# Performance work log

Hardware: AMD Instinct MI355X
Metric: run time of the kernel (lower is better)

Reference implementation:

```python
import jax, jax.numpy as jnp
import numpy as np
from jax.scipy.special import logsumexp

NUM_TAGS = 128
B, S = 256, 1024


def setup_inputs() -> dict:
    key = jax.random.key(0)
    k1, k2, k3, k4, k5 = jax.random.split(key, 5)
    emissions = jax.random.normal(k1, (B, S, NUM_TAGS), dtype=jnp.float32)
    masks = jnp.ones((B, S), dtype=jnp.float32)
    tags = jax.random.randint(k2, (B, S), 0, NUM_TAGS, dtype=jnp.int64)
    transitions = jax.random.normal(k3, (NUM_TAGS, NUM_TAGS), dtype=jnp.float32)
    start_transitions = jax.random.normal(k4, (NUM_TAGS,), dtype=jnp.float32)
    end_transitions = jax.random.normal(k5, (NUM_TAGS,), dtype=jnp.float32)
    return {"emissions": emissions, "masks": masks, "tags": tags,
            "transitions": transitions, "start_transitions": start_transitions,
            "end_transitions": end_transitions}


def _crf_loss(emissions, masks, tags, transitions, start_transitions, end_transitions):
    b, s, t = emissions.shape

    # ---- forward algorithm (log partition) ----
    def step(alpha, xs):
        emit, m = xs  # emit: (B,T), m: (B,)
        # next[b,j] = logsumexp_i(alpha[b,i] + trans[i,j] + emit[b,j])
        nxt = logsumexp(alpha[:, :, None] + transitions[None, :, :] + emit[:, None, :], axis=1)
        alpha = jnp.where(m[:, None] > 0, nxt, alpha)
        return alpha, None

    alpha0 = jnp.broadcast_to(start_transitions[None, :], (b, t))
    # note: original torch code includes i=0 in the recurrence (applies transitions
    # from start_transitions into the first emission) -- replicated faithfully.
    alpha, _ = jax.lax.scan(step, alpha0,
                            (jnp.swapaxes(emissions, 0, 1), masks.T))
    log_z = logsumexp(alpha + end_transitions[None, :], axis=1)  # (B,)

    # ---- gold sequence score (vectorized over time) ----
    bidx = jnp.arange(b)
    score = start_transitions[tags[:, 0]]
    emit_g = jnp.take_along_axis(emissions, tags[:, :, None], axis=2)[..., 0]  # (B,S)
    score = score + jnp.sum(emit_g[:, : s - 1] * masks[:, : s - 1], axis=1)
    trans_g = transitions[tags[:, : s - 1], tags[:, 1:]]  # (B,S-1)
    score = score + jnp.sum(trans_g * masks[:, 1:], axis=1)
    last_ix = jnp.maximum(jnp.sum(masks, axis=1) - 1.0, 0.0).astype(jnp.int32)
    score = score + emissions[bidx, last_ix, tags[:, -1]] * masks[:, -1]
    score = score + end_transitions[tags[:, -1]] * masks[:, -1]

    return jnp.mean(log_z - score)


def reference(emissions, masks, tags, transitions, start_transitions, end_transitions):
    return _crf_loss(emissions, masks, tags, transitions, start_transitions, end_transitions)
```

## Files before the change

kernel.cpp:

```cpp
#include <hip/hip_runtime.h>

#define NT 128
#define SEQ 1024
#define NB 256

typedef _Float16 half2v __attribute__((ext_vector_type(2)));

#define DPP_MAX_STEP(x, ctrl)                                                   \
    fmaxf((x), __builtin_bit_cast(float, __builtin_amdgcn_update_dpp(           \
        __builtin_bit_cast(int, (x)), __builtin_bit_cast(int, (x)),             \
        (ctrl), 0xf, 0xf, false)))

__device__ __forceinline__ float wave_max_dpp(float x) {
    x = DPP_MAX_STEP(x, 0x111);
    x = DPP_MAX_STEP(x, 0x112);
    x = DPP_MAX_STEP(x, 0x114);
    x = DPP_MAX_STEP(x, 0x118);
    x = DPP_MAX_STEP(x, 0x142);
    x = DPP_MAX_STEP(x, 0x143);
    return __builtin_bit_cast(float, __builtin_amdgcn_readlane(
        __builtin_bit_cast(int, x), 63));
}

#define CRF_STEP(RC, RN, MC, DO_PRE, K, BUF)                                     \
    {                                                                            \
        float mcur = MC;                                                         \
        if (DO_PRE) { RC = emp[(K) * NT]; MC = mpp[K]; }                         \
        const uint4* p4 = (const uint4*)&p_lds[BUF][ih * 32];                    \
        float A0=0.f, A1=0.f, A2=0.f, A3=0.f;                                    \
        _Pragma("unroll")                                                        \
        for (int qi = 0; qi < 8; ++qi) {                                         \
            uint4 q = p4[qi];                                                    \
            A0 = __builtin_amdgcn_fdot2(__builtin_bit_cast(half2v, q.x),         \
                                        E[4*qi+0], A0, false);                   \
            A1 = __builtin_amdgcn_fdot2(__builtin_bit_cast(half2v, q.y),         \
                                        E[4*qi+1], A1, false);                   \
            A2 = __builtin_amdgcn_fdot2(__builtin_bit_cast(half2v, q.z),         \
                                        E[4*qi+2], A2, false);                   \
            A3 = __builtin_amdgcn_fdot2(__builtin_bit_cast(half2v, q.w),         \
                                        E[4*qi+3], A3, false);                   \
        }                                                                        \
        float sv = (A0 + A1) + (A2 + A3);                                        \
        sv += __shfl_xor(sv, 32);                  \
        float v = sv * ex;                                                       \
        if (mcur > 0.0f) { cur = v; offset += offadd; }                          \
        float curo = __shfl_xor(cur, 1);        \
        if (ih == 0 && (cl & 1) == 0)                                            \
            p_lds[(BUF)^1][16*w + (cl >> 1)] = __builtin_bit_cast(unsigned int,  \
                __builtin_amdgcn_cvt_pkrtz(cur, curo));                          \
        float wm = wave_max_dpp(cur);                                            \
        if (l == 0) wmax[(BUF)^1][w] = wm;                                       \
        __syncthreads();                                                         \
        float4 wv = *(const float4*)&wmax[(BUF)^1][0];                           \
        mx = fmaxf(fmaxf(wv.x, wv.y), fmaxf(wv.z, wv.w));                        \
        inv = __builtin_amdgcn_rcpf(256.0f * mx);                                \
        offadd = __logf(mx) + 5.545177444479562f;                                \
        ex = __expf(RN) * inv;                                                   \
    }

__global__ __launch_bounds__(256, 1) void crf_scan_kernel(
    const float* __restrict__ emissions,
    const float* __restrict__ masks,
    const int*   __restrict__ tags,
    const float* __restrict__ transitions,
    const float* __restrict__ start_t,
    const float* __restrict__ end_t,
    float* __restrict__ out_per_batch)
{
    const int b   = blockIdx.x;
    const int tid = threadIdx.x;
    const int w   = tid >> 6;
    const int l   = tid & 63;
    const int cl  = l & 31;
    const int ih  = l >> 5;
    const int c   = 32 * w + cl;
    const int i0  = 64 * ih;

    __shared__ __align__(16) unsigned int p_lds[2][64];
    __shared__ __align__(16) float        wmax[2][4];
    __shared__ float redA[4], redB[4], redC[4];
    __shared__ float msk_s[SEQ];

    half2v E[32];
    #pragma unroll
    for (int r = 0; r < 32; ++r) {
        float ea = transitions[(i0 + 2*r    ) * NT + c];
        float ob = transitions[(i0 + 2*r + 1) * NT + c];
        E[r] = half2v{(_Float16)__expf(ea), (_Float16)__expf(ob)};
    }

    for (int s = tid; s < SEQ; s += 256)
        msk_s[s] = masks[b * SEQ + s];

    float cur = __expf(start_t[c]);
    float offset = 0.0f;

    {
        float curo = __shfl_xor(cur, 1);
        if (ih == 0 && (cl & 1) == 0)
            p_lds[0][16*w + (cl >> 1)] = __builtin_bit_cast(unsigned int,
                __builtin_amdgcn_cvt_pkrtz(cur, curo));
        float wm = wave_max_dpp(cur);
        if (l == 0) wmax[0][w] = wm;
    }
    __syncthreads();

    float4 wv0 = *(const float4*)&wmax[0][0];
    float mx   = fmaxf(fmaxf(wv0.x, wv0.y), fmaxf(wv0.z, wv0.w));
    float inv  = __builtin_amdgcn_rcpf(256.0f * mx);
    float offadd = __logf(mx) + 5.545177444479562f;

    const float* eb  = emissions + (size_t)b * SEQ * NT;
    const float* mkp = masks + b * SEQ;

    float ring0 = eb[(size_t)0 * NT + c];
    float ring1 = eb[(size_t)1 * NT + c];
    float ring2 = eb[(size_t)2 * NT + c];
    float ring3 = eb[(size_t)3 * NT + c];
    float mr0 = mkp[0], mr1 = mkp[1], mr2 = mkp[2], mr3 = mkp[3];

    float ex = __expf(ring0) * inv;

    const float* emp = eb + 4 * NT + c;
    const float* mpp = mkp + 4;

    for (int it = 0; it < (SEQ - 4) / 4; ++it) {
        CRF_STEP(ring0, ring1, mr0, true, 0, 0)
        CRF_STEP(ring1, ring2, mr1, true, 1, 1)
        CRF_STEP(ring2, ring3, mr2, true, 2, 0)
        CRF_STEP(ring3, ring0, mr3, true, 3, 1)
        emp += 4 * NT;
        mpp += 4;
    }
    CRF_STEP(ring0, ring1, mr0, false, 0, 0)
    CRF_STEP(ring1, ring2, mr1, false, 0, 1)
    CRF_STEP(ring2, ring3, mr2, false, 0, 0)
    CRF_STEP(ring3, ring3, mr3, false, 0, 1)

    float term = (ih == 0) ? cur * __expf(end_t[c]) : 0.0f;
    #pragma unroll
    for (int off = 32; off; off >>= 1)
        term += __shfl_xor(term, off);
    if (l == 0) redA[w] = term;

    const int tbase = b * SEQ;
    float sc = 0.0f, sm = 0.0f;
    for (int s = tid; s < SEQ; s += 256) {
        float m = msk_s[s];
        sm += m;
        if (s < SEQ - 1) {
            int tg  = tags[tbase + s];
            int tg1 = tags[tbase + s + 1];
            sc += eb[(size_t)s * NT + tg] * m;
            sc += transitions[tg * NT + tg1] * msk_s[s + 1];
        }
    }
    #pragma unroll
    for (int off = 32; off; off >>= 1) {
        sc += __shfl_xor(sc, off);
        sm += __shfl_xor(sm, off);
    }
    if (l == 0) { redB[w] = sc; redC[w] = sm; }
    __syncthreads();

    if (tid == 0) {
        float term_t = (redA[0] + redA[1]) + (redA[2] + redA[3]);
        float log_z  = offset + __logf(term_t);
        float sct    = (redB[0] + redB[1]) + (redB[2] + redB[3]);
        float smt    = (redC[0] + redC[1]) + (redC[2] + redC[3]);
        int tg0 = tags[tbase];
        int tgl = tags[tbase + SEQ - 1];
        sct += start_t[tg0];
        int last_ix = (int)fmaxf(smt - 1.0f, 0.0f);
        float ml = msk_s[SEQ - 1];
        sct += eb[(size_t)last_ix * NT + tgl] * ml;
        sct += end_t[tgl] * ml;
        out_per_batch[b] = log_z - sct;
    }
}

__global__ void crf_reduce_kernel(const float* __restrict__ pb, float* __restrict__ out)
{
    float v = pb[threadIdx.x];
    #pragma unroll
    for (int off = 32; off; off >>= 1)
        v += __shfl_xor(v, off);
    __shared__ float s4[4];
    if ((threadIdx.x & 63) == 0) s4[threadIdx.x >> 6] = v;
    __syncthreads();
    if (threadIdx.x == 0)
        out[0] = (s4[0] + s4[1] + s4[2] + s4[3]) * (1.0f / 256.0f);
}

extern "C" void kernel_launch(void* const* d_in, const int* in_sizes, int n_in,
                              void* d_out, int out_size, void* d_ws, size_t ws_size,
                              hipStream_t stream) {
    const float* emissions   = (const float*)d_in[0];
    const float* masks       = (const float*)d_in[1];
    const int*   tags        = (const int*)  d_in[2];
    const float* transitions = (const float*)d_in[3];
    const float* start_t     = (const float*)d_in[4];
    const float* end_t       = (const float*)d_in[5];
    float* per_batch = (float*)d_ws;

    crf_scan_kernel<<<NB, 256, 0, stream>>>(emissions, masks, tags, transitions,
                                            start_t, end_t, per_batch);
    crf_reduce_kernel<<<1, 256, 0, stream>>>(per_batch, (float*)d_out);
}
```

Baseline: 646.2 us.

## Use one thread per tag with fp32 packed FMA instead of fp16 dot2 split

Switches the per-step matrix-vector product from fp16 dot2 over a 256-thread block (two halves per column, combined with a cross-lane shuffle) to 128 threads, each holding its full column of exp(transitions) in fp32 and using v_pk_fma_f32. This drops the half-column shuffle, the fp16 packing of the state vector, and the 256x scaling, and it hoists the emission exp ahead of the barrier. In exchange each thread does twice the FMA work per step and holds 128 fp32 registers for transitions, so the serial critical path may get longer even though the block now has fewer waves to synchronise.

Result: slower. 979.8 us (+51.6%).

```diff
diff --git a/kernel.cpp b/kernel.cpp
--- a/kernel.cpp
+++ b/kernel.cpp
@@ -3,8 +3,6 @@
 #define NT 128
 #define SEQ 1024
 #define NB 256
-
-typedef _Float16 half2v __attribute__((ext_vector_type(2)));
 
 #define DPP_MAX_STEP(x, ctrl)                                                   \
     fmaxf((x), __builtin_bit_cast(float, __builtin_amdgcn_update_dpp(           \
@@ -22,43 +20,44 @@
         __builtin_bit_cast(int, x), 63));
 }
 
+__device__ __forceinline__ float2 pk_fma(float2 a, float2 b, float2 c) {
+    float2 d;
+    asm("v_pk_fma_f32 %0, %1, %2, %3" : "=v"(d) : "v"(a), "v"(b), "v"(c));
+    return d;
+}
+
 #define CRF_STEP(RC, RN, MC, DO_PRE, K, BUF)                                     \
     {                                                                            \
         float mcur = MC;                                                         \
         if (DO_PRE) { RC = emp[(K) * NT]; MC = mpp[K]; }                         \
-        const uint4* p4 = (const uint4*)&p_lds[BUF][ih * 32];                    \
-        float A0=0.f, A1=0.f, A2=0.f, A3=0.f;                                    \
+        float eRN = __expf(RN);               \
+        const float4* p4r = (const float4*)&p_s[BUF][0];                         \
+        float2 a0{0.f,0.f}, a1{0.f,0.f}, a2{0.f,0.f}, a3{0.f,0.f};               \
         _Pragma("unroll")                                                        \
-        for (int qi = 0; qi < 8; ++qi) {                                         \
-            uint4 q = p4[qi];                                                    \
-            A0 = __builtin_amdgcn_fdot2(__builtin_bit_cast(half2v, q.x),         \
-                                        E[4*qi+0], A0, false);                   \
-            A1 = __builtin_amdgcn_fdot2(__builtin_bit_cast(half2v, q.y),         \
-                                        E[4*qi+1], A1, false);                   \
-            A2 = __builtin_amdgcn_fdot2(__builtin_bit_cast(half2v, q.z),         \
-                                        E[4*qi+2], A2, false);                   \
-            A3 = __builtin_amdgcn_fdot2(__builtin_bit_cast(half2v, q.w),         \
-                                        E[4*qi+3], A3, false);                   \
+        for (int q = 0; q < 16; ++q) {                                           \
+            float4 Pa = p4r[2*q];                                                \
+            float4 Pb = p4r[2*q+1];                                              \
+            a0 = pk_fma(float2{Pa.x, Pa.y}, Ep[4*q+0], a0);                      \
+            a1 = pk_fma(float2{Pa.z, Pa.w}, Ep[4*q+1], a1);                      \
+            a2 = pk_fma(float2{Pb.x, Pb.y}, Ep[4*q+2], a2);                      \
+            a3 = pk_fma(float2{Pb.z, Pb.w}, Ep[4*q+3], a3);                      \
         }                                                                        \
-        float sv = (A0 + A1) + (A2 + A3);                                        \
-        sv += __shfl_xor(sv, 32);                  \
+        float sv = ((a0.x + a0.y) + (a1.x + a1.y))                               \
+                 + ((a2.x + a2.y) + (a3.x + a3.y));                              \
         float v = sv * ex;                                                       \
         if (mcur > 0.0f) { cur = v; offset += offadd; }                          \
-        float curo = __shfl_xor(cur, 1);        \
-        if (ih == 0 && (cl & 1) == 0)                                            \
-            p_lds[(BUF)^1][16*w + (cl >> 1)] = __builtin_bit_cast(unsigned int,  \
-                __builtin_amdgcn_cvt_pkrtz(cur, curo));                          \
+        p_s[(BUF)^1][c] = cur;                      \
         float wm = wave_max_dpp(cur);                                            \
         if (l == 0) wmax[(BUF)^1][w] = wm;                                       \
         __syncthreads();                                                         \
-        float4 wv = *(const float4*)&wmax[(BUF)^1][0];                           \
-        mx = fmaxf(fmaxf(wv.x, wv.y), fmaxf(wv.z, wv.w));                        \
-        inv = __builtin_amdgcn_rcpf(256.0f * mx);                                \
-        offadd = __logf(mx) + 5.545177444479562f;                                \
-        ex = __expf(RN) * inv;                                                   \
-    }
-
-__global__ __launch_bounds__(256, 1) void crf_scan_kernel(
+        float2 wv = *(const float2*)&wmax[(BUF)^1][0];                           \
+        mx = fmaxf(wv.x, wv.y);                                                  \
+        inv = __builtin_amdgcn_rcpf(mx);                                         \
+        offadd = __logf(mx);                                                     \
+        ex = eRN * inv;                                                          \
+    }
+
+__global__ __launch_bounds__(128, 1) void crf_scan_kernel(
     const float* __restrict__ emissions,
     const float* __restrict__ masks,
     const int*   __restrict__ tags,
@@ -71,44 +70,38 @@
     const int tid = threadIdx.x;
     const int w   = tid >> 6;
     const int l   = tid & 63;
-    const int cl  = l & 31;
-    const int ih  = l >> 5;
-    const int c   = 32 * w + cl;
-    const int i0  = 64 * ih;
-
-    __shared__ __align__(16) unsigned int p_lds[2][64];
-    __shared__ __align__(16) float        wmax[2][4];
-    __shared__ float redA[4], redB[4], redC[4];
+    const int c   = tid;
+
+    __shared__ __align__(16) float p_s[2][NT];
+    __shared__ __align__(16) float wmax[2][2];
+    __shared__ float redA[2], redB[2], redC[2];
     __shared__ float msk_s[SEQ];
 
-    half2v E[32];
-    #pragma unroll
-    for (int r = 0; r < 32; ++r) {
-        float ea = transitions[(i0 + 2*r    ) * NT + c];
-        float ob = transitions[(i0 + 2*r + 1) * NT + c];
-        E[r] = half2v{(_Float16)__expf(ea), (_Float16)__expf(ob)};
-    }
-
-    for (int s = tid; s < SEQ; s += 256)
+    float2 Ep[64];
+    #pragma unroll
+    for (int r = 0; r < 64; ++r) {
+        float ea = transitions[(2*r    ) * NT + c];
+        float ob = transitions[(2*r + 1) * NT + c];
+        Ep[r] = float2{__expf(ea), __expf(ob)};
+    }
+
+    for (int s = tid; s < SEQ; s += 128)
         msk_s[s] = masks[b * SEQ + s];
 
     float cur = __expf(start_t[c]);
     float offset = 0.0f;
 
+    p_s[0][c] = cur;
     {
-        float curo = __shfl_xor(cur, 1);
-        if (ih == 0 && (cl & 1) == 0)
-            p_lds[0][16*w + (cl >> 1)] = __builtin_bit_cast(unsigned int,
-                __builtin_amdgcn_cvt_pkrtz(cur, curo));
         float wm = wave_max_dpp(cur);
         if (l == 0) wmax[0][w] = wm;
     }
     __syncthreads();
 
-    float4 wv0 = *(const float4*)&wmax[0][0];
-    float mx   = fmaxf(fmaxf(wv0.x, wv0.y), fmaxf(wv0.z, wv0.w));
-    float inv  = __builtin_amdgcn_rcpf(256.0f * mx);
-    float offadd = __logf(mx) + 5.545177444479562f;
+    float2 wv0 = *(const float2*)&wmax[0][0];
+    float mx   = fmaxf(wv0.x, wv0.y);
+    float inv  = __builtin_amdgcn_rcpf(mx);
+    float offadd = __logf(mx);
 
     const float* eb  = emissions + (size_t)b * SEQ * NT;
     const float* mkp = masks + b * SEQ;
@@ -137,7 +130,7 @@
     CRF_STEP(ring2, ring3, mr2, false, 0, 0)
     CRF_STEP(ring3, ring3, mr3, false, 0, 1)
 
-    float term = (ih == 0) ? cur * __expf(end_t[c]) : 0.0f;
+    float term = cur * __expf(end_t[c]);
     #pragma unroll
     for (int off = 32; off; off >>= 1)
         term += __shfl_xor(term, off);
@@ -145,7 +138,7 @@
 
     const int tbase = b * SEQ;
     float sc = 0.0f, sm = 0.0f;
-    for (int s = tid; s < SEQ; s += 256) {
+    for (int s = tid; s < SEQ; s += 128) {
         float m = msk_s[s];
         sm += m;
         if (s < SEQ - 1) {
@@ -164,10 +157,10 @@
     __syncthreads();
 
     if (tid == 0) {
-        float term_t = (redA[0] + redA[1]) + (redA[2] + redA[3]);
+        float term_t = redA[0] + redA[1];
         float log_z  = offset + __logf(term_t);
-        float sct    = (redB[0] + redB[1]) + (redB[2] + redB[3]);
-        float smt    = (redC[0] + redC[1]) + (redC[2] + redC[3]);
+        float sct    = redB[0] + redB[1];
+        float smt    = redC[0] + redC[1];
         int tg0 = tags[tbase];
         int tgl = tags[tbase + SEQ - 1];
         sct += start_t[tg0];
@@ -203,7 +196,7 @@
     const float* end_t       = (const float*)d_in[5];
     float* per_batch = (float*)d_ws;
 
-    crf_scan_kernel<<<NB, 256, 0, stream>>>(emissions, masks, tags, transitions,
+    crf_scan_kernel<<<NB, 128, 0, stream>>>(emissions, masks, tags, transitions,
                                             start_t, end_t, per_batch);
     crf_reduce_kernel<<<1, 256, 0, stream>>>(per_batch, (float*)d_out);
 }
```
